# Performance work log

Hardware: AMD Instinct MI355X
Metric: run time of the kernel (lower is better)

Reference implementation:

```python
import jax, jax.numpy as jnp
import numpy as np

K_SIZE = 5
SIGMA_IMG = 0.2
SIGMA_VGG = 0.02
BN_EPS = 1e-5
NORM = 2.0  # 2 * len(GPU_IDS), assuming 1 device


def _window_shifts(x, k):
    # x: (n, C, H, W) -> (n, C, H, W, k*k) neighbor values for every offset in
    # the k x k window, zero-padded at image borders.
    r = k // 2
    n, C, H, W = x.shape
    xp = jnp.pad(x, ((0, 0), (0, 0), (r, r), (r, r)))
    cols = [xp[:, :, di:di + H, dj:dj + W] for di in range(k) for dj in range(k)]
    return jnp.stack(cols, axis=-1)


def _modularity(img, seg, k, sigma):
    # img: (n, C, H, W) feature map; seg: (n, K, H, W) soft assignments.
    n, K, H, W = seg.shape
    seg2 = _window_shifts(seg, k)                                  # (n,K,H,W,kk)
    img2 = _window_shifts(img, k)                                  # (n,C,H,W,kk)
    valid = _window_shifts(jnp.ones((1, 1, H, W), img.dtype), k)[:, 0]  # (1,H,W,kk)
    d2 = ((img[..., None] - img2) ** 2).sum(axis=1)                # (n,H,W,kk)
    w12 = jax.lax.stop_gradient(jnp.exp(-d2 / (2.0 * sigma * sigma)) * valid)
    # numerator: sum over pixels & pairs of p1*p2*w12, per (n, K)
    num = jnp.einsum('nkhw,nkhwp,nhwp->nk', seg, seg2, w12)
    # p1 (sum over pairs of p1/n_pairs) == seg; w1 = sum over pairs of w12
    w1 = w12.sum(axis=-1)                                          # (n,H,W)
    den = jnp.einsum('nhw,nkhw->nk', w1, seg)
    rel = num / den                                                # (n,K)
    return rel.sum(axis=1) / (K * n)                               # (n,)


def _conv(x, w, b):
    y = jax.lax.conv_general_dilated(x, w, (1, 1), 'SAME',
                                     dimension_numbers=('NCHW', 'OIHW', 'NCHW'))
    return y + b[None, :, None, None]


def _maxpool2(x):
    return jax.lax.reduce_window(x, -jnp.inf, jax.lax.max,
                                 (1, 1, 2, 2), (1, 1, 2, 2), 'VALID')


def _avgpool2(x):
    n, c, h, w = x.shape
    return x.reshape(n, c, h // 2, 2, w // 2, 2).mean(axis=(3, 5))


def _vgg8(x, w1, b1, w2, b2, w3, b3, w4, b4):
    # VGG16 features[:8]: conv1_1, conv1_2, maxpool, conv2_1, conv2_2 (relu each)
    x = jax.nn.relu(_conv(x, w1, b1))
    x = jax.nn.relu(_conv(x, w2, b2))
    x = _maxpool2(x)
    x = jax.nn.relu(_conv(x, w3, b3))
    x = jax.nn.relu(_conv(x, w4, b4))
    return x


def _batchnorm(x):
    # fresh BatchNorm2d in training mode (weight=1, bias=0), then detach
    m = x.mean(axis=(0, 2, 3), keepdims=True)
    v = x.var(axis=(0, 2, 3), keepdims=True)
    return jax.lax.stop_gradient((x - m) / jnp.sqrt(v + BN_EPS))


def setup_inputs() -> dict:
    key = jax.random.key(0)
    ks = jax.random.split(key, 6)
    images = jax.random.uniform(ks[0], (4, 3, 128, 128), jnp.float32)
    seg = jax.random.uniform(ks[1], (4, 8, 128, 128), jnp.float32)
    segmentation = seg / seg.sum(axis=1, keepdims=True)
    w1 = jax.random.normal(ks[2], (64, 3, 3, 3), jnp.float32) * 0.1
    w2 = jax.random.normal(ks[3], (64, 64, 3, 3), jnp.float32) * 0.05
    w3 = jax.random.normal(ks[4], (128, 64, 3, 3), jnp.float32) * 0.05
    w4 = jax.random.normal(ks[5], (128, 128, 3, 3), jnp.float32) * 0.03
    return {'images': images, 'segmentation': segmentation,
            'w1': w1, 'b1': jnp.zeros(64), 'w2': w2, 'b2': jnp.zeros(64),
            'w3': w3, 'b3': jnp.zeros(128), 'w4': w4, 'b4': jnp.zeros(128)}


def reference(images, segmentation, w1, b1, w2, b2, w3, b3, w4, b4):
    fich = _batchnorm(_vgg8(images, w1, b1, w2, b2, w3, b3, w4, b4))  # (n,128,64,64)
    images_n = _batchnorm(images)
    down_seg = segmentation
    while down_seg.shape[-1] != fich.shape[-1]:
        down_seg = _avgpool2(down_seg)
    loss = (_modularity(fich, down_seg, K_SIZE, SIGMA_VGG).sum()
            + _modularity(images_n, segmentation, K_SIZE, SIGMA_IMG).sum())
    return loss / NORM
```

## Files before the change

kernel.cpp:

```cpp
#include <hip/hip_runtime.h>
#include <hip/hip_bf16.h>
#include <math.h>

typedef __attribute__((ext_vector_type(8))) short short8;
typedef __attribute__((ext_vector_type(4))) float floatx4;
typedef unsigned short ushortT;

__device__ inline short f2bf(float v) {
    __hip_bfloat16 h = __float2bfloat16(v);
    union { __hip_bfloat16 h; short s; } u; u.h = h; return u.s;
}
__device__ inline void gstore(float* p, float v) {
    __hip_atomic_store(p, v, __ATOMIC_RELAXED, __HIP_MEMORY_SCOPE_AGENT);
}
__device__ inline float gload(const float* p) {
    return __hip_atomic_load(p, __ATOMIC_RELAXED, __HIP_MEMORY_SCOPE_AGENT);
}

#define OFF_C2    0
#define OFF_PAD4  8388608
#define OFF_FICH  12849152
#define OFF_PAD2  21237760
#define OFF_PAD3  29890560
#define OFF_WP2   32120832
#define OFF_WP3   32194560
#define OFF_WP4   32342016
#define OFF_CNT   33947648
#define OFF_P64   33951744
#define OFF_P128  33968128
#define OFF_PBN   34033664
#define OFF_PIMG  34295808

__global__ __launch_bounds__(256) void prologue(
    char* ws, const float* __restrict__ images,
    const float* __restrict__ w1, const float* __restrict__ b1,
    const float* __restrict__ w2, const float* __restrict__ w3,
    const float* __restrict__ w4)
{
    __shared__ float plds[3 * 720];
    __shared__ float rs[256], rs2[256];

    int b = blockIdx.x;
    int tid = threadIdx.x;

    if (b == 0 && tid == 0) *(int*)(ws + OFF_CNT) = 0;

    if (b >= 1362) {
        int bid = b - 1362;
        int txt = bid & 7; bid >>= 3;
        int tyt = bid & 7; bid >>= 3;
        int ocg = bid & 7; bid >>= 3;
        int n = bid;
        int x0 = txt * 16, y0 = tyt * 16;
        int tx = tid & 15, ty = tid >> 4;
        short* outp = (short*)(ws + OFF_PAD2);

        for (int i = tid; i < 972; i += 256) {
            int cc = i / 324; int rem = i - cc * 324;
            int r = rem / 18, c = rem - r * 18;
            int y = y0 - 1 + r, x = x0 - 1 + c;
            float v = 0.f;
            if ((unsigned)y < 128u && (unsigned)x < 128u)
                v = images[((size_t)(n * 3 + cc) * 128 + y) * 128 + x];
            plds[cc * 720 + r * 40 + c] = v;
        }
        __syncthreads();

        float acc[8];
#pragma unroll
        for (int oc = 0; oc < 8; ++oc) acc[oc] = 0.f;
        const float* w_g = w1 + (size_t)(ocg * 8) * 27;
#pragma unroll
        for (int cc = 0; cc < 3; ++cc) {
            const float* base = &plds[cc * 720 + ty * 40 + tx];
            float i00 = base[0],  i01 = base[1],  i02 = base[2];
            float i10 = base[40], i11 = base[41], i12 = base[42];
            float i20 = base[80], i21 = base[81], i22 = base[82];
            const float* wp = w_g + cc * 9;
#pragma unroll
            for (int oc = 0; oc < 8; ++oc) {
                const float* wq = wp + oc * 27;
                float a = acc[oc];
                a = fmaf(wq[0], i00, a); a = fmaf(wq[1], i01, a); a = fmaf(wq[2], i02, a);
                a = fmaf(wq[3], i10, a); a = fmaf(wq[4], i11, a); a = fmaf(wq[5], i12, a);
                a = fmaf(wq[6], i20, a); a = fmaf(wq[7], i21, a); a = fmaf(wq[8], i22, a);
                acc[oc] = a;
            }
        }
        int oy = y0 + ty, ox = x0 + tx;
        short* o = outp + ((size_t)(n * 130 + oy + 1) * 130 + ox + 1) * 64 + ocg * 8;
#pragma unroll
        for (int oc = 0; oc < 8; ++oc) {
            float v = fmaxf(acc[oc] + b1[ocg * 8 + oc], 0.f);
            o[oc] = f2bf(v);
        }
        return;
    }

    if (b < 162) {
        int t = b * 256 + tid;
        short* base; int Hp, Wp, C; int idx;
        if (t < 16512)      { base = (short*)(ws + OFF_PAD2); Hp = 130; Wp = 130; C = 64;  idx = t; }
        else if (t < 24832) { base = (short*)(ws + OFF_PAD3); Hp = 66;  Wp = 66;  C = 64;  idx = t - 16512; }
        else if (t < 41472) { base = (short*)(ws + OFF_PAD4); Hp = 66;  Wp = 66;  C = 128; idx = t - 24832; }
        else return;
        int c8 = idx % (C / 8); int rest = idx / (C / 8);
        int haloPx = 2 * Wp + 2 * (Hp - 2);
        int p = rest % haloPx; int n = rest / haloPx;
        int y, x;
        if (p < Wp)          { y = 0;      x = p; }
        else if (p < 2 * Wp) { y = Hp - 1; x = p - Wp; }
        else { int j = p - 2 * Wp; y = 1 + (j >> 1); x = (j & 1) ? (Wp - 1) : 0; }
        short8 z = {0, 0, 0, 0, 0, 0, 0, 0};
        *(short8*)&base[((size_t)((n * Hp + y) * Wp) + x) * C + c8 * 8] = z;
        return;
    }
    if (b < 1170) {
        int e = (b - 162) * 256 + tid;
        const float* w; short* wp; int CIN, NTALL;
        if (e < 36864)       { w = w2; wp = (short*)(ws + OFF_WP2); CIN = 64;  NTALL = 4; }
        else if (e < 110592) { e -= 36864;  w = w3; wp = (short*)(ws + OFF_WP3); CIN = 64;  NTALL = 8; }
        else if (e < 258048) { e -= 110592; w = w4; wp = (short*)(ws + OFF_WP4); CIN = 128; NTALL = 8; }
        else return;
        int j = e & 7; int L = (e >> 3) & 63; int rest = e >> 9;
        int nt = rest % NTALL; int rest2 = rest / NTALL;
        int KT = CIN / 32;
        int kt = rest2 % KT; int t = rest2 / KT;
        int oc = nt * 16 + (L & 15);
        int ci = kt * 32 + (L >> 4) * 8 + j;
        wp[e] = f2bf(w[((size_t)oc * CIN + ci) * 9 + t]);
        return;
    }
    {
        float* part = (float*)(ws + OFF_PIMG);
        int bb = b - 1170;
        int c = bb >> 6, chunk = bb & 63;
        int base = chunk * 1024 + tid;
        float s = 0.f, s2 = 0.f;
#pragma unroll
        for (int k = 0; k < 4; ++k) {
            int i = base + k * 256;
            int n = i >> 14, hw = i & 16383;
            float v = images[(((size_t)(n * 3 + c)) << 14) + hw];
            s += v; s2 = fmaf(v, v, s2);
        }
        rs[tid] = s; rs2[tid] = s2;
        __syncthreads();
        for (int k = 128; k > 0; k >>= 1) {
            if (tid < k) { rs[tid] += rs[tid + k]; rs2[tid] += rs2[tid + k]; }
            __syncthreads();
        }
        if (tid == 0) { part[bb * 2] = rs[0]; part[bb * 2 + 1] = rs2[0]; }
    }
}

__global__ __launch_bounds__(256) void conv2_pool(
    const short* __restrict__ inp,
    const short* __restrict__ wp,
    const float* __restrict__ bias,
    short* __restrict__ outp)
{
    constexpr int CIN = 64;
    constexpr int Hp = 130, Wp = 130;

    int bid = blockIdx.x;
    int o2 = bid & 1; bid >>= 1;
    int xt = bid & 1; bid >>= 1;
    int yq = bid & 31; bid >>= 5;
    int n = bid;
    int y0 = yq * 4;
    int x0 = xt * 64;

    int tid = threadIdx.x;
    int wv = tid >> 6, lane = tid & 63;
    int lm = lane & 15, q = lane >> 4;
    int px0 = x0 + 16 * wv;
    int ntb = o2 * 2;

    floatx4 acc[4][2];
#pragma unroll
    for (int d = 0; d < 4; ++d)
#pragma unroll
        for (int t = 0; t < 2; ++t) acc[d][t] = (floatx4){0.f, 0.f, 0.f, 0.f};

    const short* a_m = inp + lm * CIN + q * 8;
    const short* wbase = wp + ((size_t)ntb * 64 + lane) * 8;

    for (int kt = 0; kt < 2; ++kt) {
        int kofs = kt * 32;
#pragma unroll
        for (int s = 0; s < 3; ++s) {
            const short* acol = a_m + ((size_t)((n * Hp + y0) * Wp) + px0 + s) * CIN + kofs;
            short8 av[6];
#pragma unroll
            for (int j = 0; j < 6; ++j)
                av[j] = *(const short8*)(acol + (size_t)j * Wp * CIN);
#pragma unroll
            for (int r = 0; r < 3; ++r) {
                const short* bp = wbase + (size_t)(((r * 3 + s) * 2 + kt) * 4) * 512;
                short8 b0 = *(const short8*)bp;
                short8 b1 = *(const short8*)(bp + 512);
#pragma unroll
                for (int d = 0; d < 4; ++d) {
                    acc[d][0] = __builtin_amdgcn_mfma_f32_16x16x32_bf16(av[r + d], b0, acc[d][0], 0, 0, 0);
                    acc[d][1] = __builtin_amdgcn_mfma_f32_16x16x32_bf16(av[r + d], b1, acc[d][1], 0, 0, 0);
                }
            }
        }
    }

    int ox = (px0 + q * 4) >> 1;
#pragma unroll
    for (int t2 = 0; t2 < 2; ++t2) {
        int oc = (ntb + t2) * 16 + lm;
        float bs = bias[oc];
#pragma unroll
        for (int p = 0; p < 2; ++p) {
            float v00 = fmaxf(acc[2 * p][t2][0] + bs, 0.f);
            float v01 = fmaxf(acc[2 * p][t2][1] + bs, 0.f);
            float v02 = fmaxf(acc[2 * p][t2][2] + bs, 0.f);
            float v03 = fmaxf(acc[2 * p][t2][3] + bs, 0.f);
            float v10 = fmaxf(acc[2 * p + 1][t2][0] + bs, 0.f);
            float v11 = fmaxf(acc[2 * p + 1][t2][1] + bs, 0.f);
            float v12 = fmaxf(acc[2 * p + 1][t2][2] + bs, 0.f);
            float v13 = fmaxf(acc[2 * p + 1][t2][3] + bs, 0.f);
            float m0 = fmaxf(fmaxf(v00, v01), fmaxf(v10, v11));
            float m1 = fmaxf(fmaxf(v02, v03), fmaxf(v12, v13));
            int oy = yq * 2 + p;
            short* o = outp + ((size_t)(n * 66 + oy + 1) * 66 + ox + 1) * 64 + oc;
            o[0]  = f2bf(m0);
            o[64] = f2bf(m1);
        }
    }
}

__global__ __launch_bounds__(256) void conv3_2row(
    const short* __restrict__ inp,
    const short* __restrict__ wp,
    const float* __restrict__ bias,
    short* __restrict__ outp)
{
    constexpr int CIN = 64, COUT = 128, Hp = 66, Wp = 66, KT = 2, NTALL = 8;

    int bid = blockIdx.x;
    int bn = bid & 3; bid >>= 2;
    int yq = bid & 31; bid >>= 5;
    int n = bid;
    int y0 = yq * 2;

    int tid = threadIdx.x;
    int wv = tid >> 6, lane = tid & 63;
    int lm = lane & 15, q = lane >> 4;
    int px0 = 16 * wv;
    int ntb = bn * 2;

    floatx4 acc[2][2];
#pragma unroll
    for (int d = 0; d < 2; ++d)
#pragma unroll
        for (int t = 0; t < 2; ++t) acc[d][t] = (floatx4){0.f, 0.f, 0.f, 0.f};

    const short* a_m = inp + lm * CIN + q * 8;
    const short* wbase = wp + ((size_t)ntb * 64 + lane) * 8;

    for (int kt = 0; kt < KT; ++kt) {
        int kofs = kt * 32;
#pragma unroll
        for (int s = 0; s < 3; ++s) {
            const short* acol = a_m + ((size_t)((n * Hp + y0) * Wp) + px0 + s) * CIN + kofs;
            short8 av[4];
#pragma unroll
            for (int j = 0; j < 4; ++j)
                av[j] = *(const short8*)(acol + (size_t)j * Wp * CIN);
#pragma unroll
            for (int r = 0; r < 3; ++r) {
                const short* bp = wbase + (size_t)(((r * 3 + s) * KT + kt) * NTALL) * 512;
                short8 b0 = *(const short8*)bp;
                short8 b1 = *(const short8*)(bp + 512);
#pragma unroll
                for (int d = 0; d < 2; ++d) {
                    acc[d][0] = __builtin_amdgcn_mfma_f32_16x16x32_bf16(av[r + d], b0, acc[d][0], 0, 0, 0);
                    acc[d][1] = __builtin_amdgcn_mfma_f32_16x16x32_bf16(av[r + d], b1, acc[d][1], 0, 0, 0);
                }
            }
        }
    }

#pragma unroll
    for (int t2 = 0; t2 < 2; ++t2) {
        int oc = (ntb + t2) * 16 + lm;
        float bs = bias[oc];
#pragma unroll
        for (int d = 0; d < 2; ++d) {
#pragma unroll
            for (int i = 0; i < 4; ++i) {
                int px = px0 + q * 4 + i;
                float v = fmaxf(acc[d][t2][i] + bs, 0.f);
                outp[((size_t)(n * Hp + y0 + d + 1) * Wp + px + 1) * COUT + oc] = f2bf(v);
            }
        }
    }
}

__global__ __launch_bounds__(256) void conv4_bn(
    const short* __restrict__ inp,
    const short* __restrict__ wp,
    const float* __restrict__ bias,
    float* __restrict__ out,
    float* __restrict__ part)
{
    constexpr int CIN = 128, Hp = 66, Wp = 66, KT = 4, NTALL = 8;

    int bid = blockIdx.x;
    int bn = bid & 3; bid >>= 2;
    int yq = bid & 31; bid >>= 5;
    int n = bid;
    int y0 = yq * 2;

    int tid = threadIdx.x;
    int wv = tid >> 6, lane = tid & 63;
    int lm = lane & 15, q = lane >> 4;
    int px0 = 16 * wv;
    int ntb = bn * 2;

    floatx4 acc[2][2];
#pragma unroll
    for (int d = 0; d < 2; ++d)
#pragma unroll
        for (int t = 0; t < 2; ++t) acc[d][t] = (floatx4){0.f, 0.f, 0.f, 0.f};

    const short* a_m = inp + lm * CIN + q * 8;
    const short* wbase = wp + ((size_t)ntb * 64 + lane) * 8;

    for (int kt = 0; kt < KT; ++kt) {
        int kofs = kt * 32;
#pragma unroll
        for (int s = 0; s < 3; ++s) {
            const short* acol = a_m + ((size_t)((n * Hp + y0) * Wp) + px0 + s) * CIN + kofs;
            short8 av[4];
#pragma unroll
            for (int j = 0; j < 4; ++j)
                av[j] = *(const short8*)(acol + (size_t)j * Wp * CIN);
#pragma unroll
            for (int r = 0; r < 3; ++r) {
                const short* bp = wbase + (size_t)(((r * 3 + s) * KT + kt) * NTALL) * 512;
                short8 b0 = *(const short8*)bp;
                short8 b1 = *(const short8*)(bp + 512);
#pragma unroll
                for (int d = 0; d < 2; ++d) {
                    acc[d][0] = __builtin_amdgcn_mfma_f32_16x16x32_bf16(av[r + d], b0, acc[d][0], 0, 0, 0);
                    acc[d][1] = __builtin_amdgcn_mfma_f32_16x16x32_bf16(av[r + d], b1, acc[d][1], 0, 0, 0);
                }
            }
        }
    }

    __shared__ float ps[4][2][16], ps2[4][2][16];
#pragma unroll
    for (int t2 = 0; t2 < 2; ++t2) {
        int oc = (ntb + t2) * 16 + lm;
        float bs = bias[oc];
        float sv = 0.f, sv2 = 0.f;
#pragma unroll
        for (int d = 0; d < 2; ++d) {
#pragma unroll
            for (int i = 0; i < 4; ++i) {
                int px = px0 + q * 4 + i;
                float v = fmaxf(acc[d][t2][i] + bs, 0.f);
                out[((size_t)(n * 64 + y0 + d) * 64 + px) * 128 + oc] = v;
                sv += v; sv2 = fmaf(v, v, sv2);
            }
        }
        sv  += __shfl_xor(sv, 16, 64);  sv  += __shfl_xor(sv, 32, 64);
        sv2 += __shfl_xor(sv2, 16, 64); sv2 += __shfl_xor(sv2, 32, 64);
        if (q == 0) { ps[wv][t2][lm] = sv; ps2[wv][t2][lm] = sv2; }
    }
    __syncthreads();
    if (tid < 32) {
        int t_ = tid >> 4, lm_ = tid & 15;
        float a  = ps[0][t_][lm_] + ps[1][t_][lm_] + ps[2][t_][lm_] + ps[3][t_][lm_];
        float a2 = ps2[0][t_][lm_] + ps2[1][t_][lm_] + ps2[2][t_][lm_] + ps2[3][t_][lm_];
        part[(size_t)blockIdx.x * 64 + tid * 2]     = a;
        part[(size_t)blockIdx.x * 64 + tid * 2 + 1] = a2;
    }
}

__device__ __forceinline__ void mod64_body(
    int obid,
    const float* __restrict__ xt, const float* __restrict__ seg,
    const float* __restrict__ pbn, float* __restrict__ part,
    float* fl, float (*sl)[12][14], float* stf)
{
    int tid = threadIdx.x;
    int w = tid >> 6, lane = tid & 63;
    int tx = lane & 7, ty = lane >> 3;
    int bid = obid;
    int bx = bid & 7; bid >>= 3;
    int by = bid & 7; bid >>= 3;
    int n = bid;
    int x0 = bx * 8, y0 = by * 8;

    for (int i = tid; i < 8 * 144; i += 256) {
        int k = i / 144;
        int rem = i - k * 144;
        int r = rem / 12, c = rem - r * 12;
        int y = y0 - 2 + r, x = x0 - 2 + c;
        float v = 0.f;
        if ((unsigned)y < 64u && (unsigned)x < 64u) {
            const float* p = seg + ((size_t)(n * 8 + k) * 128 + 2 * y) * 128 + 2 * x;
            float2 a = *(const float2*)p;
            float2 b = *(const float2*)(p + 128);
            v = 0.25f * ((a.x + a.y) + (b.x + b.y));
        }
        sl[k][r][c] = v;
    }

    {
        int c = tid & 127, h = tid >> 7;
        int bnq = c >> 5, lc = c & 31;
        float s = 0.f, s2 = 0.f;
        const float* pb = pbn + lc * 2;
        for (int i = 0; i < 64; ++i) {
            int b = (h * 64 + i) * 4 + bnq;
            float2 v = *(const float2*)(pb + (size_t)b * 64);
            s += v.x; s2 += v.y;
        }
        fl[tid] = s; fl[256 + tid] = s2;
        __syncthreads();
        if (tid < 128) {
            float ss = fl[tid] + fl[tid + 128];
            float qq = fl[256 + tid] + fl[256 + tid + 128];
            float mean = ss * (1.f / 16384.f);
            float var = qq * (1.f / 16384.f) - mean * mean;
            stf[tid] = 1.f / sqrtf(var + 1e-5f);
        }
        __syncthreads();
    }

    float* slab = fl + w * 2880;

    float d2p[25];
#pragma unroll
    for (int di = 0; di < 5; ++di)
#pragma unroll
        for (int dj = 0; dj < 5; ++dj) {
            int y2 = y0 + ty + di - 2, x2 = x0 + tx + dj - 2;
            float bias = ((unsigned)y2 < 64u && (unsigned)x2 < 64u) ? 0.f : 1e30f;
            d2p[di * 5 + dj] = (w == 0) ? bias : 0.f;
        }

    for (int r8 = 0; r8 < 2; ++r8) {
        int ch0 = w * 32 + r8 * 16;
        for (int i = lane; i < 576; i += 64) {
            int pix = i >> 2, q = i & 3;
            int r = pix / 12, c = pix - r * 12;
            int y = y0 - 2 + r, x = x0 - 2 + c;
            float4 v = make_float4(0.f, 0.f, 0.f, 0.f);
            if ((unsigned)y < 64u && (unsigned)x < 64u) {
                v = *(const float4*)&xt[((size_t)((n * 64 + y) * 64 + x)) * 128 + ch0 + q * 4];
                float4 sv = *(const float4*)&stf[ch0 + q * 4];
                v.x *= sv.x; v.y *= sv.y; v.z *= sv.z; v.w *= sv.w;
            }
            *(float4*)&slab[(r * 12 + c) * 20 + q * 4] = v;
        }

        const float* ctr = &slab[((ty + 2) * 12 + tx + 2) * 20];
        float4 c0 = *(const float4*)(ctr + 0);
        float4 c1 = *(const float4*)(ctr + 4);
        float4 c2 = *(const float4*)(ctr + 8);
        float4 c3 = *(const float4*)(ctr + 12);
#pragma unroll
        for (int di = 0; di < 5; ++di)
#pragma unroll
            for (int dj = 0; dj < 5; ++dj) {
                const float* np = &slab[((ty + di) * 12 + tx + dj) * 20];
                float4 v0 = *(const float4*)(np + 0);
                float4 v1 = *(const float4*)(np + 4);
                float4 v2 = *(const float4*)(np + 8);
                float4 v3 = *(const float4*)(np + 12);
                float d = d2p[di * 5 + dj];
                float e;
                e = c0.x - v0.x; d = fmaf(e, e, d);
                e = c0.y - v0.y; d = fmaf(e, e, d);
                e = c0.z - v0.z; d = fmaf(e, e, d);
                e = c0.w - v0.w; d = fmaf(e, e, d);
                e = c1.x - v1.x; d = fmaf(e, e, d);
                e = c1.y - v1.y; d = fmaf(e, e, d);
                e = c1.z - v1.z; d = fmaf(e, e, d);
                e = c1.w - v1.w; d = fmaf(e, e, d);
                e = c2.x - v2.x; d = fmaf(e, e, d);
                e = c2.y - v2.y; d = fmaf(e, e, d);
                e = c2.z - v2.z; d = fmaf(e, e, d);
                e = c2.w - v2.w; d = fmaf(e, e, d);
                e = c3.x - v3.x; d = fmaf(e, e, d);
                e = c3.y - v3.y; d = fmaf(e, e, d);
                e = c3.z - v3.z; d = fmaf(e, e, d);
                e = c3.w - v3.w; d = fmaf(e, e, d);
                d2p[di * 5 + dj] = d;
            }
    }

#pragma unroll
    for (int j = 0; j < 25; ++j) slab[lane * 25 + j] = d2p[j];
    __syncthreads();

    const float minus_inv2s2 = -1.0f / (2.0f * 0.02f * 0.02f);
    for (int i = tid; i < 1600; i += 256) {
        float d = fl[i] + fl[2880 + i] + fl[5760 + i] + fl[8640 + i];
        fl[i] = expf(d * minus_inv2s2);
    }
    __syncthreads();

    float wgt[25];
    float w1 = 0.f;
#pragma unroll
    for (int j = 0; j < 25; ++j) { wgt[j] = fl[lane * 25 + j]; w1 += wgt[j]; }
#pragma unroll
    for (int kk = 0; kk < 2; ++kk) {
        int k = w * 2 + kk;
        float s = 0.f;
#pragma unroll
        for (int di = 0; di < 5; ++di)
#pragma unroll
            for (int dj = 0; dj < 5; ++dj)
                s = fmaf(wgt[di * 5 + dj], sl[k][ty + di][tx + dj], s);
        float sc = sl[k][ty + 2][tx + 2];
        float numk = s * sc;
        float denk = w1 * sc;
#pragma unroll
        for (int sh = 32; sh > 0; sh >>= 1) {
            numk += __shfl_xor(numk, sh, 64);
            denk += __shfl_xor(denk, sh, 64);
        }
        if (lane == 0) {
            gstore(&part[(size_t)obid * 16 + k * 2], numk);
            gstore(&part[(size_t)obid * 16 + k * 2 + 1], denk);
        }
    }
}

__device__ __forceinline__ void mod128_body(
    int obid,
    const float* __restrict__ img, const float* __restrict__ pimg,
    const float* __restrict__ seg, float* __restrict__ part,
    float (*il)[12][4], float (*sl)[12][14], float* stm)
{
    int t = threadIdx.x;
    int w = t >> 6, lane = t & 63;
    int tx = lane & 7, ty = lane >> 3;

    if (t < 64) {
#pragma unroll
        for (int ch = 0; ch < 3; ++ch) {
            float s  = pimg[(ch * 64 + t) * 2];
            float s2 = pimg[(ch * 64 + t) * 2 + 1];
#pragma unroll
            for (int sh = 32; sh > 0; sh >>= 1) {
                s += __shfl_xor(s, sh, 64);
                s2 += __shfl_xor(s2, sh, 64);
            }
            if (t == 0) {
                float mean = s * (1.f / 65536.f);
                float var = s2 * (1.f / 65536.f) - mean * mean;
                stm[ch] = mean;
                stm[3 + ch] = 1.f / sqrtf(var + 1e-5f);
            }
        }
    }

    int bid = obid;
    int bx = bid & 15; bid >>= 4;
    int by = bid & 15; bid >>= 4;
    int n = bid;
    int x0 = bx * 8, y0 = by * 8;

    for (int i = t; i < 8 * 144; i += 256) {
        int k = i / 144;
        int rem = i - k * 144;
        int r = rem / 12, c = rem - r * 12;
        int y = y0 - 2 + r, x = x0 - 2 + c;
        float v = 0.f;
        if ((unsigned)y < 128u && (unsigned)x < 128u)
            v = seg[((size_t)(n * 8 + k) * 128 + y) * 128 + x];
        sl[k][r][c] = v;
    }
    __syncthreads();

    float mn0 = stm[0], mn1 = stm[1], mn2 = stm[2];
    float rs0 = stm[3], rs1 = stm[4], rs2 = stm[5];

    for (int i = t; i < 432; i += 256) {
        int ch = i / 144; int pix = i - ch * 144;
        int r = pix / 12, c = pix - r * 12;
        int y = y0 - 2 + r, x = x0 - 2 + c;
        float v = 0.f;
        if ((unsigned)y < 128u && (unsigned)x < 128u) {
            float raw = img[(((size_t)(n * 3 + ch)) << 14) + y * 128 + x];
            float mn = ch == 0 ? mn0 : (ch == 1 ? mn1 : mn2);
            float rs = ch == 0 ? rs0 : (ch == 1 ? rs1 : rs2);
            v = (raw - mn) * rs;
        }
        il[r][c][ch] = v;
    }
    __syncthreads();

    const float minus_inv2s2 = -1.0f / (2.0f * 0.2f * 0.2f);
    float c0 = il[ty + 2][tx + 2][0];
    float c1 = il[ty + 2][tx + 2][1];
    float c2 = il[ty + 2][tx + 2][2];

    float wgt[25];
    float w1 = 0.f;
#pragma unroll
    for (int di = 0; di < 5; ++di)
#pragma unroll
        for (int dj = 0; dj < 5; ++dj) {
            int y2 = y0 + ty + di - 2, x2 = x0 + tx + dj - 2;
            float bias = ((unsigned)y2 < 128u && (unsigned)x2 < 128u) ? 0.f : 1e30f;
            const float* np = &il[ty + di][tx + dj][0];
            float e0 = c0 - np[0], e1 = c1 - np[1], e2 = c2 - np[2];
            float d = bias + fmaf(e2, e2, fmaf(e1, e1, e0 * e0));
            float wv = __expf(d * minus_inv2s2);
            wgt[di * 5 + dj] = wv;
            w1 += wv;
        }

#pragma unroll
    for (int kk = 0; kk < 2; ++kk) {
        int k = w * 2 + kk;
        float s = 0.f;
#pragma unroll
        for (int di = 0; di < 5; ++di)
#pragma unroll
            for (int dj = 0; dj < 5; ++dj)
                s = fmaf(wgt[di * 5 + dj], sl[k][ty + di][tx + dj], s);
        float sc = sl[k][ty + 2][tx + 2];
        float numk = s * sc;
        float denk = w1 * sc;
#pragma unroll
        for (int sft = 32; sft > 0; sft >>= 1) {
            numk += __shfl_xor(numk, sft, 64);
            denk += __shfl_xor(denk, sft, 64);
        }
        if (lane == 0) {
            gstore(&part[(size_t)obid * 16 + k * 2], numk);
            gstore(&part[(size_t)obid * 16 + k * 2 + 1], denk);
        }
    }
}

__global__ __launch_bounds__(256) void modularity_all(
    const float* __restrict__ xt,
    const float* __restrict__ seg,
    const float* __restrict__ pbn,
    const float* __restrict__ img,
    const float* __restrict__ pimg,
    float* __restrict__ p64, float* __restrict__ p128,
    float* __restrict__ out, int* __restrict__ cnt)
{
    __shared__ float fl[4 * 2880];
    __shared__ float sl[8][12][14];
    __shared__ float stm[6];
    __shared__ __align__(16) float stf[128];
    __shared__ int lastf;

    int bid = blockIdx.x;
    int tid = threadIdx.x;
    int g = bid / 5;
    int r5 = bid - g * 5;
    if (r5 == 0) {
        mod64_body(g, xt, seg, pbn, p64, fl, sl, stf);
    } else {
        mod128_body(bid - g - 1, img, pimg, seg, p128,
                    (float(*)[12][4])fl, sl, stm);
    }

    __syncthreads();
    if (tid == 0) {
        int old = __hip_atomic_fetch_add(cnt, 1, __ATOMIC_ACQ_REL, __HIP_MEMORY_SCOPE_AGENT);
        lastf = (old == 1279);
    }
    __syncthreads();
    if (!lastf) return;

    int j = tid >> 2, s4 = tid & 3;
    float num = 0.f, den = 0.f;
    if (j < 32) {
        int n = j >> 3, k = j & 7;
        for (int i = 0; i < 16; ++i) {
            int b = s4 * 16 + i;
            const float* p = p64 + ((size_t)(n * 64 + b)) * 16 + k * 2;
            num += gload(p); den += gload(p + 1);
        }
    } else {
        int jj = j - 32; int n = jj >> 3, k = jj & 7;
        for (int i = 0; i < 64; ++i) {
            int b = s4 * 64 + i;
            const float* p = p128 + ((size_t)(n * 256 + b)) * 16 + k * 2;
            num += gload(p); den += gload(p + 1);
        }
    }
    num += __shfl_xor(num, 1, 64); den += __shfl_xor(den, 1, 64);
    num += __shfl_xor(num, 2, 64); den += __shfl_xor(den, 2, 64);
    if (s4 == 0) { fl[j] = num; fl[64 + j] = den; }
    __syncthreads();
    if (tid < 64) {
        float v = fl[tid] / fl[64 + tid];
#pragma unroll
        for (int sh = 32; sh > 0; sh >>= 1) v += __shfl_xor(v, sh, 64);
        if (tid == 0) out[0] = v * (1.0f / 64.0f);
    }
}

extern "C" void kernel_launch(void* const* d_in, const int* in_sizes, int n_in,
                              void* d_out, int out_size, void* d_ws, size_t ws_size,
                              hipStream_t stream)
{
    const float* images = (const float*)d_in[0];
    const float* seg    = (const float*)d_in[1];
    const float* w1 = (const float*)d_in[2]; const float* b1 = (const float*)d_in[3];
    const float* w2 = (const float*)d_in[4]; const float* b2 = (const float*)d_in[5];
    const float* w3 = (const float*)d_in[6]; const float* b3 = (const float*)d_in[7];
    const float* w4 = (const float*)d_in[8]; const float* b4 = (const float*)d_in[9];
    float* out = (float*)d_out;
    char* ws = (char*)d_ws;
    short* PAD2 = (short*)(ws + OFF_PAD2);
    short* PAD3 = (short*)(ws + OFF_PAD3);
    short* PAD4 = (short*)(ws + OFF_PAD4);
    float* FICH = (float*)(ws + OFF_FICH);
    short* WP2  = (short*)(ws + OFF_WP2);
    short* WP3  = (short*)(ws + OFF_WP3);
    short* WP4  = (short*)(ws + OFF_WP4);
    float* P64  = (float*)(ws + OFF_P64);
    float* P128 = (float*)(ws + OFF_P128);
    float* PBN  = (float*)(ws + OFF_PBN);
    float* PIMG = (float*)(ws + OFF_PIMG);
    int*   CNT  = (int*)(ws + OFF_CNT);

    prologue<<<3410, 256, 0, stream>>>(ws, images, w1, b1, w2, w3, w4);
    conv2_pool<<<512, 256, 0, stream>>>(PAD2, WP2, b2, PAD3);
    conv3_2row<<<512, 256, 0, stream>>>(PAD3, WP3, b3, PAD4);
    conv4_bn<<<512, 256, 0, stream>>>(PAD4, WP4, b4, FICH, PBN);
    modularity_all<<<1280, 256, 0, stream>>>(FICH, seg, PBN, images, PIMG,
                                             P64, P128, out, CNT);
}
```

Measured before the change: 192.3 us.

## Fuse image-modularity into conv3 launch and split final reduction into kernels

Moves the 128x128 image modularity blocks out of the final kernel and appends them as extra blocks of the conv3 launch, so that independent work can fill idle CUs alongside the conv. The final stage is split into a BN-statistics finalize kernel, a 64x64 feature modularity kernel, and a single-block reduction. This replaces the atomic last-block counter and the per-block redundant BN stat recomputation. It adds two extra kernel launches, and the conv3 launch gets larger shared-memory usage and register pressure from the merged body.

```diff
diff --git a/kernel.cpp b/kernel.cpp
--- a/kernel.cpp
+++ b/kernel.cpp
@@ -9,12 +9,6 @@
 __device__ inline short f2bf(float v) {
     __hip_bfloat16 h = __float2bfloat16(v);
     union { __hip_bfloat16 h; short s; } u; u.h = h; return u.s;
-}
-__device__ inline void gstore(float* p, float v) {
-    __hip_atomic_store(p, v, __ATOMIC_RELAXED, __HIP_MEMORY_SCOPE_AGENT);
-}
-__device__ inline float gload(const float* p) {
-    return __hip_atomic_load(p, __ATOMIC_RELAXED, __HIP_MEMORY_SCOPE_AGENT);
 }
 
 #define OFF_C2    0
@@ -25,7 +19,7 @@
 #define OFF_WP2   32120832
 #define OFF_WP3   32194560
 #define OFF_WP4   32342016
-#define OFF_CNT   33947648
+#define OFF_ST    33947648
 #define OFF_P64   33951744
 #define OFF_P128  33968128
 #define OFF_PBN   34033664
@@ -42,8 +36,6 @@
 
     int b = blockIdx.x;
     int tid = threadIdx.x;
-
-    if (b == 0 && tid == 0) *(int*)(ws + OFF_CNT) = 0;
 
     if (b >= 1362) {
         int bid = b - 1362;
@@ -234,12 +226,135 @@
     }
 }
 
-__global__ __launch_bounds__(256) void conv3_2row(
+__device__ __forceinline__ void mod128_body(
+    int obid,
+    const float* __restrict__ img, const float* __restrict__ pimg,
+    const float* __restrict__ seg, float* __restrict__ part,
+    float (*il)[12][4], float (*sl)[12][14], float* stm)
+{
+    int t = threadIdx.x;
+    int w = t >> 6, lane = t & 63;
+    int tx = lane & 7, ty = lane >> 3;
+
+    if (t < 64) {
+#pragma unroll
+        for (int ch = 0; ch < 3; ++ch) {
+            float s  = pimg[(ch * 64 + t) * 2];
+            float s2 = pimg[(ch * 64 + t) * 2 + 1];
+#pragma unroll
+            for (int sh = 32; sh > 0; sh >>= 1) {
+                s += __shfl_xor(s, sh, 64);
+                s2 += __shfl_xor(s2, sh, 64);
+            }
+            if (t == 0) {
+                float mean = s * (1.f / 65536.f);
+                float var = s2 * (1.f / 65536.f) - mean * mean;
+                stm[ch] = mean;
+                stm[3 + ch] = 1.f / sqrtf(var + 1e-5f);
+            }
+        }
+    }
+
+    int bid = obid;
+    int bx = bid & 15; bid >>= 4;
+    int by = bid & 15; bid >>= 4;
+    int n = bid;
+    int x0 = bx * 8, y0 = by * 8;
+
+    for (int i = t; i < 8 * 144; i += 256) {
+        int k = i / 144;
+        int rem = i - k * 144;
+        int r = rem / 12, c = rem - r * 12;
+        int y = y0 - 2 + r, x = x0 - 2 + c;
+        float v = 0.f;
+        if ((unsigned)y < 128u && (unsigned)x < 128u)
+            v = seg[((size_t)(n * 8 + k) * 128 + y) * 128 + x];
+        sl[k][r][c] = v;
+    }
+    __syncthreads();
+
+    float mn0 = stm[0], mn1 = stm[1], mn2 = stm[2];
+    float rs0 = stm[3], rs1 = stm[4], rs2 = stm[5];
+
+    for (int i = t; i < 432; i += 256) {
+        int ch = i / 144; int pix = i - ch * 144;
+        int r = pix / 12, c = pix - r * 12;
+        int y = y0 - 2 + r, x = x0 - 2 + c;
+        float v = 0.f;
+        if ((unsigned)y < 128u && (unsigned)x < 128u) {
+            float raw = img[(((size_t)(n * 3 + ch)) << 14) + y * 128 + x];
+            float mn = ch == 0 ? mn0 : (ch == 1 ? mn1 : mn2);
+            float rs = ch == 0 ? rs0 : (ch == 1 ? rs1 : rs2);
+            v = (raw - mn) * rs;
+        }
+        il[r][c][ch] = v;
+    }
+    __syncthreads();
+
+    const float minus_inv2s2 = -1.0f / (2.0f * 0.2f * 0.2f);
+    float c0 = il[ty + 2][tx + 2][0];
+    float c1 = il[ty + 2][tx + 2][1];
+    float c2 = il[ty + 2][tx + 2][2];
+
+    float wgt[25];
+    float w1 = 0.f;
+#pragma unroll
+    for (int di = 0; di < 5; ++di)
+#pragma unroll
+        for (int dj = 0; dj < 5; ++dj) {
+            int y2 = y0 + ty + di - 2, x2 = x0 + tx + dj - 2;
+            float bias = ((unsigned)y2 < 128u && (unsigned)x2 < 128u) ? 0.f : 1e30f;
+            const float* np = &il[ty + di][tx + dj][0];
+            float e0 = c0 - np[0], e1 = c1 - np[1], e2 = c2 - np[2];
+            float d = bias + fmaf(e2, e2, fmaf(e1, e1, e0 * e0));
+            float wv = __expf(d * minus_inv2s2);
+            wgt[di * 5 + dj] = wv;
+            w1 += wv;
+        }
+
+#pragma unroll
+    for (int kk = 0; kk < 2; ++kk) {
+        int k = w * 2 + kk;
+        float s = 0.f;
+#pragma unroll
+        for (int di = 0; di < 5; ++di)
+#pragma unroll
+            for (int dj = 0; dj < 5; ++dj)
+                s = fmaf(wgt[di * 5 + dj], sl[k][ty + di][tx + dj], s);
+        float sc = sl[k][ty + 2][tx + 2];
+        float numk = s * sc;
+        float denk = w1 * sc;
+#pragma unroll
+        for (int sft = 32; sft > 0; sft >>= 1) {
+            numk += __shfl_xor(numk, sft, 64);
+            denk += __shfl_xor(denk, sft, 64);
+        }
+        if (lane == 0) {
+            part[(size_t)obid * 16 + k * 2] = numk;
+            part[(size_t)obid * 16 + k * 2 + 1] = denk;
+        }
+    }
+}
+
+__global__ __launch_bounds__(256) void conv3_mod128(
     const short* __restrict__ inp,
     const short* __restrict__ wp,
     const float* __restrict__ bias,
-    short* __restrict__ outp)
-{
+    short* __restrict__ outp,
+    const float* __restrict__ img,
+    const float* __restrict__ pimg,
+    const float* __restrict__ seg,
+    float* __restrict__ p128)
+{
+    __shared__ float il[12][12][4];
+    __shared__ float sl[8][12][14];
+    __shared__ float stm[6];
+
+    if (blockIdx.x >= 512) {
+        mod128_body(blockIdx.x - 512, img, pimg, seg, p128, il, sl, stm);
+        return;
+    }
+
     constexpr int CIN = 64, COUT = 128, Hp = 66, Wp = 66, KT = 2, NTALL = 8;
 
     int bid = blockIdx.x;
@@ -385,15 +500,42 @@
     }
 }
 
-__device__ __forceinline__ void mod64_body(
-    int obid,
-    const float* __restrict__ xt, const float* __restrict__ seg,
-    const float* __restrict__ pbn, float* __restrict__ part,
-    float* fl, float (*sl)[12][14], float* stf)
-{
+__global__ __launch_bounds__(256) void stats_fin(const float* __restrict__ part,
+                                                 float* __restrict__ st)
+{
+    int ch = blockIdx.x;
+    int t = threadIdx.x;
+    int bn = ch >> 5, lc = ch & 31;
+    __shared__ float rs[128], rs2[128];
+    if (t < 128) {
+        const float* p = part + ((size_t)(t * 4 + bn)) * 64 + lc * 2;
+        rs[t] = p[0]; rs2[t] = p[1];
+    }
+    __syncthreads();
+    for (int k = 64; k > 0; k >>= 1) {
+        if (t < k) { rs[t] += rs[t + k]; rs2[t] += rs2[t + k]; }
+        __syncthreads();
+    }
+    if (t == 0) {
+        float mean = rs[0] * (1.f / 16384.f);
+        float var = rs2[0] * (1.f / 16384.f) - mean * mean;
+        st[ch] = 1.f / sqrtf(var + 1e-5f);
+    }
+}
+
+__global__ __launch_bounds__(256) void modularity64(
+    const float* __restrict__ xt,
+    const float* __restrict__ seg,
+    const float* __restrict__ st,
+    float* __restrict__ part)
+{
+    __shared__ float fl[4 * 2880];
+    __shared__ float sl[8][12][14];
+
     int tid = threadIdx.x;
     int w = tid >> 6, lane = tid & 63;
     int tx = lane & 7, ty = lane >> 3;
+    int obid = blockIdx.x;
     int bid = obid;
     int bx = bid & 7; bid >>= 3;
     int by = bid & 7; bid >>= 3;
@@ -415,28 +557,6 @@
         sl[k][r][c] = v;
     }
 
-    {
-        int c = tid & 127, h = tid >> 7;
-        int bnq = c >> 5, lc = c & 31;
-        float s = 0.f, s2 = 0.f;
-        const float* pb = pbn + lc * 2;
-        for (int i = 0; i < 64; ++i) {
-            int b = (h * 64 + i) * 4 + bnq;
-            float2 v = *(const float2*)(pb + (size_t)b * 64);
-            s += v.x; s2 += v.y;
-        }
-        fl[tid] = s; fl[256 + tid] = s2;
-        __syncthreads();
-        if (tid < 128) {
-            float ss = fl[tid] + fl[tid + 128];
-            float qq = fl[256 + tid] + fl[256 + tid + 128];
-            float mean = ss * (1.f / 16384.f);
-            float var = qq * (1.f / 16384.f) - mean * mean;
-            stf[tid] = 1.f / sqrtf(var + 1e-5f);
-        }
-        __syncthreads();
-    }
-
     float* slab = fl + w * 2880;
 
     float d2p[25];
@@ -458,7 +578,7 @@
             float4 v = make_float4(0.f, 0.f, 0.f, 0.f);
             if ((unsigned)y < 64u && (unsigned)x < 64u) {
                 v = *(const float4*)&xt[((size_t)((n * 64 + y) * 64 + x)) * 128 + ch0 + q * 4];
-                float4 sv = *(const float4*)&stf[ch0 + q * 4];
+                float4 sv = *(const float4*)&st[ch0 + q * 4];
                 v.x *= sv.x; v.y *= sv.y; v.z *= sv.z; v.w *= sv.w;
             }
             *(float4*)&slab[(r * 12 + c) * 20 + q * 4] = v;
@@ -533,182 +653,49 @@
             denk += __shfl_xor(denk, sh, 64);
         }
         if (lane == 0) {
-            gstore(&part[(size_t)obid * 16 + k * 2], numk);
-            gstore(&part[(size_t)obid * 16 + k * 2 + 1], denk);
-        }
-    }
-}
-
-__device__ __forceinline__ void mod128_body(
-    int obid,
-    const float* __restrict__ img, const float* __restrict__ pimg,
-    const float* __restrict__ seg, float* __restrict__ part,
-    float (*il)[12][4], float (*sl)[12][14], float* stm)
+            part[(size_t)obid * 16 + k * 2] = numk;
+            part[(size_t)obid * 16 + k * 2 + 1] = denk;
+        }
+    }
+}
+
+__global__ __launch_bounds__(1024) void reduce_finalize(
+    const float* __restrict__ p64, const float* __restrict__ p128,
+    float* __restrict__ out)
 {
     int t = threadIdx.x;
-    int w = t >> 6, lane = t & 63;
-    int tx = lane & 7, ty = lane >> 3;
-
-    if (t < 64) {
-#pragma unroll
-        for (int ch = 0; ch < 3; ++ch) {
-            float s  = pimg[(ch * 64 + t) * 2];
-            float s2 = pimg[(ch * 64 + t) * 2 + 1];
-#pragma unroll
-            for (int sh = 32; sh > 0; sh >>= 1) {
-                s += __shfl_xor(s, sh, 64);
-                s2 += __shfl_xor(s2, sh, 64);
-            }
-            if (t == 0) {
-                float mean = s * (1.f / 65536.f);
-                float var = s2 * (1.f / 65536.f) - mean * mean;
-                stm[ch] = mean;
-                stm[3 + ch] = 1.f / sqrtf(var + 1e-5f);
-            }
-        }
-    }
-
-    int bid = obid;
-    int bx = bid & 15; bid >>= 4;
-    int by = bid & 15; bid >>= 4;
-    int n = bid;
-    int x0 = bx * 8, y0 = by * 8;
-
-    for (int i = t; i < 8 * 144; i += 256) {
-        int k = i / 144;
-        int rem = i - k * 144;
-        int r = rem / 12, c = rem - r * 12;
-        int y = y0 - 2 + r, x = x0 - 2 + c;
-        float v = 0.f;
-        if ((unsigned)y < 128u && (unsigned)x < 128u)
-            v = seg[((size_t)(n * 8 + k) * 128 + y) * 128 + x];
-        sl[k][r][c] = v;
-    }
-    __syncthreads();
-
-    float mn0 = stm[0], mn1 = stm[1], mn2 = stm[2];
-    float rs0 = stm[3], rs1 = stm[4], rs2 = stm[5];
-
-    for (int i = t; i < 432; i += 256) {
-        int ch = i / 144; int pix = i - ch * 144;
-        int r = pix / 12, c = pix - r * 12;
-        int y = y0 - 2 + r, x = x0 - 2 + c;
-        float v = 0.f;
-        if ((unsigned)y < 128u && (unsigned)x < 128u) {
-            float raw = img[(((size_t)(n * 3 + ch)) << 14) + y * 128 + x];
-            float mn = ch == 0 ? mn0 : (ch == 1 ? mn1 : mn2);
-            float rs = ch == 0 ? rs0 : (ch == 1 ? rs1 : rs2);
-            v = (raw - mn) * rs;
-        }
-        il[r][c][ch] = v;
-    }
-    __syncthreads();
-
-    const float minus_inv2s2 = -1.0f / (2.0f * 0.2f * 0.2f);
-    float c0 = il[ty + 2][tx + 2][0];
-    float c1 = il[ty + 2][tx + 2][1];
-    float c2 = il[ty + 2][tx + 2][2];
-
-    float wgt[25];
-    float w1 = 0.f;
-#pragma unroll
-    for (int di = 0; di < 5; ++di)
-#pragma unroll
-        for (int dj = 0; dj < 5; ++dj) {
-            int y2 = y0 + ty + di - 2, x2 = x0 + tx + dj - 2;
-            float bias = ((unsigned)y2 < 128u && (unsigned)x2 < 128u) ? 0.f : 1e30f;
-            const float* np = &il[ty + di][tx + dj][0];
-            float e0 = c0 - np[0], e1 = c1 - np[1], e2 = c2 - np[2];
-            float d = bias + fmaf(e2, e2, fmaf(e1, e1, e0 * e0));
-            float wv = __expf(d * minus_inv2s2);
-            wgt[di * 5 + dj] = wv;
-            w1 += wv;
-        }
-
-#pragma unroll
-    for (int kk = 0; kk < 2; ++kk) {
-        int k = w * 2 + kk;
-        float s = 0.f;
-#pragma unroll
-        for (int di = 0; di < 5; ++di)
-#pragma unroll
-            for (int dj = 0; dj < 5; ++dj)
-                s = fmaf(wgt[di * 5 + dj], sl[k][ty + di][tx + dj], s);
-        float sc = sl[k][ty + 2][tx + 2];
-        float numk = s * sc;
-        float denk = w1 * sc;
-#pragma unroll
-        for (int sft = 32; sft > 0; sft >>= 1) {
-            numk += __shfl_xor(numk, sft, 64);
-            denk += __shfl_xor(denk, sft, 64);
-        }
-        if (lane == 0) {
-            gstore(&part[(size_t)obid * 16 + k * 2], numk);
-            gstore(&part[(size_t)obid * 16 + k * 2 + 1], denk);
-        }
-    }
-}
-
-__global__ __launch_bounds__(256) void modularity_all(
-    const float* __restrict__ xt,
-    const float* __restrict__ seg,
-    const float* __restrict__ pbn,
-    const float* __restrict__ img,
-    const float* __restrict__ pimg,
-    float* __restrict__ p64, float* __restrict__ p128,
-    float* __restrict__ out, int* __restrict__ cnt)
-{
-    __shared__ float fl[4 * 2880];
-    __shared__ float sl[8][12][14];
-    __shared__ float stm[6];
-    __shared__ __align__(16) float stf[128];
-    __shared__ int lastf;
-
-    int bid = blockIdx.x;
-    int tid = threadIdx.x;
-    int g = bid / 5;
-    int r5 = bid - g * 5;
-    if (r5 == 0) {
-        mod64_body(g, xt, seg, pbn, p64, fl, sl, stf);
-    } else {
-        mod128_body(bid - g - 1, img, pimg, seg, p128,
-                    (float(*)[12][4])fl, sl, stm);
-    }
-
-    __syncthreads();
-    if (tid == 0) {
-        int old = __hip_atomic_fetch_add(cnt, 1, __ATOMIC_ACQ_REL, __HIP_MEMORY_SCOPE_AGENT);
-        lastf = (old == 1279);
-    }
-    __syncthreads();
-    if (!lastf) return;
-
-    int j = tid >> 2, s4 = tid & 3;
+    int j = t >> 4, s = t & 15;
     float num = 0.f, den = 0.f;
     if (j < 32) {
         int n = j >> 3, k = j & 7;
-        for (int i = 0; i < 16; ++i) {
-            int b = s4 * 16 + i;
+#pragma unroll
+        for (int i = 0; i < 4; ++i) {
+            int b = s * 4 + i;
             const float* p = p64 + ((size_t)(n * 64 + b)) * 16 + k * 2;
-            num += gload(p); den += gload(p + 1);
+            num += p[0]; den += p[1];
         }
     } else {
         int jj = j - 32; int n = jj >> 3, k = jj & 7;
-        for (int i = 0; i < 64; ++i) {
-            int b = s4 * 64 + i;
+#pragma unroll
+        for (int i = 0; i < 16; ++i) {
+            int b = s * 16 + i;
             const float* p = p128 + ((size_t)(n * 256 + b)) * 16 + k * 2;
-            num += gload(p); den += gload(p + 1);
-        }
-    }
-    num += __shfl_xor(num, 1, 64); den += __shfl_xor(den, 1, 64);
-    num += __shfl_xor(num, 2, 64); den += __shfl_xor(den, 2, 64);
-    if (s4 == 0) { fl[j] = num; fl[64 + j] = den; }
+            num += p[0]; den += p[1];
+        }
+    }
+#pragma unroll
+    for (int sh = 8; sh > 0; sh >>= 1) {
+        num += __shfl_xor(num, sh, 16);
+        den += __shfl_xor(den, sh, 16);
+    }
+    __shared__ float rn[64], rd[64];
+    if (s == 0) { rn[j] = num; rd[j] = den; }
     __syncthreads();
-    if (tid < 64) {
-        float v = fl[tid] / fl[64 + tid];
+    if (t < 64) {
+        float v = rn[t] / rd[t];
 #pragma unroll
         for (int sh = 32; sh > 0; sh >>= 1) v += __shfl_xor(v, sh, 64);
-        if (tid == 0) out[0] = v * (1.0f / 64.0f);
+        if (t == 0) out[0] = v * (1.0f / 64.0f);
     }
 }
 
@@ -731,16 +718,18 @@
     short* WP2  = (short*)(ws + OFF_WP2);
     short* WP3  = (short*)(ws + OFF_WP3);
     short* WP4  = (short*)(ws + OFF_WP4);
+    float* ST   = (float*)(ws + OFF_ST);
     float* P64  = (float*)(ws + OFF_P64);
     float* P128 = (float*)(ws + OFF_P128);
     float* PBN  = (float*)(ws + OFF_PBN);
     float* PIMG = (float*)(ws + OFF_PIMG);
-    int*   CNT  = (int*)(ws + OFF_CNT);
 
     prologue<<<3410, 256, 0, stream>>>(ws, images, w1, b1, w2, w3, w4);
     conv2_pool<<<512, 256, 0, stream>>>(PAD2, WP2, b2, PAD3);
-    conv3_2row<<<512, 256, 0, stream>>>(PAD3, WP3, b3, PAD4);
+    conv3_mod128<<<1536, 256, 0, stream>>>(PAD3, WP3, b3, PAD4,
+                                           images, PIMG, seg, P128);
     conv4_bn<<<512, 256, 0, stream>>>(PAD4, WP4, b4, FICH, PBN);
-    modularity_all<<<1280, 256, 0, stream>>>(FICH, seg, PBN, images, PIMG,
-                                             P64, P128, out, CNT);
-}
+    stats_fin<<<128, 256, 0, stream>>>(PBN, ST);
+    modularity64<<<256, 256, 0, stream>>>(FICH, seg, ST, P64);
+    reduce_finalize<<<1, 1024, 0, stream>>>(P64, P128, out);
+}
```

Result: faster. 162.6 us (-15.4%).
